# Kernel optimization log

Hardware: AMD Instinct MI355X
Metric: run time of the kernel (lower is better)

The kernel has to match this reference:

```python
import jax, jax.numpy as jnp
import numpy as np

B, T, D, H = 4, 2048, 1024, 64

def setup_inputs() -> dict:
    key = jax.random.key(0)
    kx, kq, kk, kv = jax.random.split(key, 4)
    s = 1.0 / np.sqrt(D)
    return {
        "x": jax.random.normal(kx, (B, T, D), dtype=jnp.float32),
        "Wq": jax.random.normal(kq, (D, H), dtype=jnp.float32) * s,
        "Wk": jax.random.normal(kk, (D, H), dtype=jnp.float32) * s,
        "Wv": jax.random.normal(kv, (D, H), dtype=jnp.float32) * s,
    }

def reference(x, Wq, Wk, Wv):
    # q,k,v: [B,T,H]
    q = jnp.einsum('btd,dh->bth', x, Wq)
    k = jnp.einsum('btd,dh->bth', x, Wk)
    v = jnp.einsum('btd,dh->bth', x, Wv)
    scale = jnp.asarray(H, x.dtype) ** -0.5
    wei = jnp.einsum('bqh,bkh->bqk', q, k) * scale  # [B,T,T]
    Tlen = x.shape[1]
    causal = jnp.tril(jnp.ones((Tlen, Tlen), dtype=bool))
    wei = jnp.where(causal, wei, -jnp.inf)
    attn = jax.nn.softmax(wei, axis=-1)
    return jnp.einsum('bqk,bkh->bqh', attn, v)
```

## Files before the change

### kernel.cpp

```cpp
#include <hip/hip_runtime.h>
#include <hip/hip_bf16.h>
#include <math.h>

#define Bb   4
#define Tlen 2048
#define Dd   1024
#define Hh   64
#define NROWS 8192
#define NQ   32
#define NC   4

typedef short bf16x8 __attribute__((ext_vector_type(8)));
typedef float f32x4  __attribute__((ext_vector_type(4)));

__device__ __forceinline__ unsigned short f2b(float f) {
    unsigned u = __float_as_uint(f);
    unsigned r = u + 0x7FFFu + ((u >> 16) & 1u);
    return (unsigned short)(r >> 16);
}
__device__ __forceinline__ unsigned pk2(float a, float b) {
    __hip_bfloat162 h = __float22bfloat162_rn(make_float2(a, b));
    return *reinterpret_cast<unsigned*>(&h);
}

__global__ __launch_bounds__(256) void wtrans_kernel(
    const float* __restrict__ Wq, const float* __restrict__ Wk,
    const float* __restrict__ Wv, unsigned short* __restrict__ wfrag)
{
    const int s = blockIdx.x * 256 + threadIdx.x;
    const int f   = s / 768;
    const int rem = s % 768;
    const int nb  = rem >> 6;
    const int lane = rem & 63;
    const int g = lane >> 4, qr = lane & 15;
    const int n = nb * 16 + qr;
    const int wsel = n >> 6, h = n & 63;
    const float* W = (wsel == 0) ? Wq : (wsel == 1) ? Wk : Wv;
    const int k0 = (f >> 1) * 64 + (f & 1) * 32 + g * 8;
    unsigned short tmp[8];
    #pragma unroll
    for (int j = 0; j < 8; ++j) tmp[j] = f2b(W[(size_t)(k0 + j) * Hh + h]);
    *(bf16x8*)(wfrag + (size_t)s * 8) = *(const bf16x8*)tmp;
}

__global__ __launch_bounds__(256) void proj_kernel(
    const float* __restrict__ x, const unsigned short* __restrict__ wfrag,
    unsigned short* __restrict__ qw, unsigned short* __restrict__ kw,
    unsigned short* __restrict__ vw)
{
    __shared__ unsigned short xs[2][32 * 64];

    const int rb   = blockIdx.x * 32;
    const int tid  = threadIdx.x;
    const int wv   = tid >> 6;
    const int lane = tid & 63;
    const int qr   = lane & 15;
    const int g    = lane >> 4;

    const int xr = tid >> 3, xc8 = tid & 7;
    const float* xg0 = x + (size_t)(rb + xr) * Dd + xc8 * 8;

    const unsigned short* wp = wfrag + ((size_t)(wv * 3) * 64 + lane) * 8;

    f32x4 acc[6] = {};

    float4 px0 = *(const float4*)(xg0 + 0);
    float4 px1 = *(const float4*)(xg0 + 4);

    #pragma unroll
    for (int t = 0; t < 16; ++t) {
        const int cur = t & 1;
        {
            union { unsigned u[4]; bf16x8 v; } p8;
            p8.u[0] = pk2(px0.x, px0.y);
            p8.u[1] = pk2(px0.z, px0.w);
            p8.u[2] = pk2(px1.x, px1.y);
            p8.u[3] = pk2(px1.z, px1.w);
            *(bf16x8*)(&xs[cur][xr * 64 + ((xc8 ^ (xr & 7)) << 3)]) = p8.v;
        }
        __syncthreads();

        if (t < 15) {
            px0 = *(const float4*)(xg0 + (t + 1) * 64 + 0);
            px1 = *(const float4*)(xg0 + (t + 1) * 64 + 4);
        }

        #pragma unroll
        for (int ks = 0; ks < 2; ++ks) {
            const int f = t * 2 + ks;
            bf16x8 b0 = *(const bf16x8*)(wp + (size_t)(f * 12 + 0) * 512);
            bf16x8 b1 = *(const bf16x8*)(wp + (size_t)(f * 12 + 1) * 512);
            bf16x8 b2 = *(const bf16x8*)(wp + (size_t)(f * 12 + 2) * 512);
            #pragma unroll
            for (int mf = 0; mf < 2; ++mf) {
                const int arow = mf * 16 + qr;
                const bf16x8 a = *(const bf16x8*)(
                    &xs[cur][arow * 64 + (((ks * 4 + g) ^ (arow & 7)) << 3)]);
                acc[mf * 3 + 0] = __builtin_amdgcn_mfma_f32_16x16x32_bf16(a, b0, acc[mf * 3 + 0], 0, 0, 0);
                acc[mf * 3 + 1] = __builtin_amdgcn_mfma_f32_16x16x32_bf16(a, b1, acc[mf * 3 + 1], 0, 0, 0);
                acc[mf * 3 + 2] = __builtin_amdgcn_mfma_f32_16x16x32_bf16(a, b2, acc[mf * 3 + 2], 0, 0, 0);
            }
        }
        __syncthreads();
    }

    #pragma unroll
    for (int mf = 0; mf < 2; ++mf) {
        #pragma unroll
        for (int nf = 0; nf < 3; ++nf) {
            const int n = wv * 48 + nf * 16 + qr;
            const int wsel = n >> 6, h = n & 63;
            unsigned short* out = (wsel == 0) ? qw : (wsel == 1) ? kw : vw;
            const f32x4 ov = acc[mf * 3 + nf];
            #pragma unroll
            for (int r = 0; r < 4; ++r)
                out[(size_t)(rb + mf * 16 + 4 * g + r) * Hh + h] = f2b(ov[r]);
        }
    }
}

#define XSTR 72
#define VSTR 40
__global__ __launch_bounds__(256) void attn_kernel(
    const unsigned short* __restrict__ qw, const unsigned short* __restrict__ kw,
    const unsigned short* __restrict__ vw,
    float* __restrict__ part_O, float* __restrict__ part_ml)
{
    __shared__ unsigned short ks_s[32 * XSTR];
    __shared__ unsigned short vt_s[64 * VSTR];

    const int qt = (NQ - 1) - blockIdx.x;
    const int ci = blockIdx.y;
    const int b  = blockIdx.z;
    const int tid = threadIdx.x;
    const int wv = tid >> 6, lane = tid & 63;
    const int qr = lane & 15, g = lane >> 4;

    const int ntk = 2 * qt + 2;
    const int tpc = (ntk + NC - 1) / NC;
    const int t0  = ci * tpc;
    const int t1  = (ntk < t0 + tpc) ? ntk : (t0 + tpc);

    const size_t base = (size_t)b * Tlen * Hh;
    const int qrow = qt * 64 + wv * 16 + qr;

    const bf16x8 qf0 = *(const bf16x8*)(qw + base + (size_t)qrow * Hh + 8 * g);
    const bf16x8 qf1 = *(const bf16x8*)(qw + base + (size_t)qrow * Hh + 32 + 8 * g);

    f32x4 o0 = {}, o1 = {}, o2 = {}, o3 = {};
    float m = -INFINITY, l = 0.f;

    for (int kt = t0; kt < t1; ++kt) {
        const int j0 = kt * 32;
        __syncthreads();
        {
            const int row = tid >> 3, cg = tid & 7;
            const bf16x8 k8 = *(const bf16x8*)(kw + base + (size_t)(j0 + row) * Hh + cg * 8);
            *(bf16x8*)(&ks_s[row * XSTR + ((cg ^ (row & 3)) << 3)]) = k8;
            const bf16x8 v8 = *(const bf16x8*)(vw + base + (size_t)(j0 + row) * Hh + cg * 8);
            #pragma unroll
            for (int u = 0; u < 8; ++u) {
                const int c = cg * 8 + u;
                const int jx = row ^ (((c >> 3) & 3) << 3);
                vt_s[c * VSTR + jx] = ((const unsigned short*)&v8)[u];
            }
        }
        __syncthreads();

        f32x4 a0 = {}, a1 = {};
        {
            const int sw = (g ^ (qr & 3)) << 3;
            bf16x8 kf;
            kf = *(const bf16x8*)(&ks_s[qr * XSTR + sw]);
            a0 = __builtin_amdgcn_mfma_f32_16x16x32_bf16(kf, qf0, a0, 0, 0, 0);
            kf = *(const bf16x8*)(&ks_s[qr * XSTR + 32 + sw]);
            a0 = __builtin_amdgcn_mfma_f32_16x16x32_bf16(kf, qf1, a0, 0, 0, 0);
            kf = *(const bf16x8*)(&ks_s[(16 + qr) * XSTR + sw]);
            a1 = __builtin_amdgcn_mfma_f32_16x16x32_bf16(kf, qf0, a1, 0, 0, 0);
            kf = *(const bf16x8*)(&ks_s[(16 + qr) * XSTR + 32 + sw]);
            a1 = __builtin_amdgcn_mfma_f32_16x16x32_bf16(kf, qf1, a1, 0, 0, 0);
        }

        float p[8];
        float tm = -INFINITY;
        #pragma unroll
        for (int jf = 0; jf < 2; ++jf) {
            #pragma unroll
            for (int r = 0; r < 4; ++r) {
                const int jg = j0 + jf * 16 + 4 * g + r;
                float s = ((jf == 0) ? a0[r] : a1[r]) * 0.125f;
                s = (jg > qrow) ? -INFINITY : s;
                p[jf * 4 + r] = s;
                tm = fmaxf(tm, s);
            }
        }
        tm = fmaxf(tm, __shfl_xor(tm, 16));
        tm = fmaxf(tm, __shfl_xor(tm, 32));
        const float mnew  = fmaxf(m, tm);
        const float alpha = (m == -INFINITY) ? 0.f : __expf(m - mnew);
        float psum = 0.f;
        #pragma unroll
        for (int i = 0; i < 8; ++i) {
            const float pv = (p[i] == -INFINITY) ? 0.f : __expf(p[i] - mnew);
            p[i] = pv; psum += pv;
        }
        psum += __shfl_xor(psum, 16);
        psum += __shfl_xor(psum, 32);
        l = l * alpha + psum;
        m = mnew;

        const float ar0 = __shfl(alpha, 4 * g + 0);
        const float ar1 = __shfl(alpha, 4 * g + 1);
        const float ar2 = __shfl(alpha, 4 * g + 2);
        const float ar3 = __shfl(alpha, 4 * g + 3);
        o0[0] *= ar0; o0[1] *= ar1; o0[2] *= ar2; o0[3] *= ar3;
        o1[0] *= ar0; o1[1] *= ar1; o1[2] *= ar2; o1[3] *= ar3;
        o2[0] *= ar0; o2[1] *= ar1; o2[2] *= ar2; o2[3] *= ar3;
        o3[0] *= ar0; o3[1] *= ar1; o3[2] *= ar2; o3[3] *= ar3;

        unsigned pw[4];
        pw[0] = f2b(p[0]) | ((unsigned)f2b(p[1]) << 16);
        pw[1] = f2b(p[2]) | ((unsigned)f2b(p[3]) << 16);
        pw[2] = f2b(p[4]) | ((unsigned)f2b(p[5]) << 16);
        pw[3] = f2b(p[6]) | ((unsigned)f2b(p[7]) << 16);
        union PU { unsigned u[4]; bf16x8 v; } pu;
        #pragma unroll
        for (int w = 0; w < 4; ++w) {
            const int gp  = 2 * g + (w >> 1);
            const int src = 16 * (gp & 3) + qr;
            const unsigned t0s = __shfl(pw[0 + (w & 1)], src);
            const unsigned t1s = __shfl(pw[2 + (w & 1)], src);
            pu.u[w] = (gp & 4) ? t1s : t0s;
        }
        const bf16x8 pa = pu.v;

        {
            int cb = qr;
            bf16x8 vf = *(const bf16x8*)(&vt_s[cb * VSTR + 8 * (g ^ ((cb >> 3) & 3))]);
            o0 = __builtin_amdgcn_mfma_f32_16x16x32_bf16(pa, vf, o0, 0, 0, 0);
            cb = 16 + qr;
            vf = *(const bf16x8*)(&vt_s[cb * VSTR + 8 * (g ^ ((cb >> 3) & 3))]);
            o1 = __builtin_amdgcn_mfma_f32_16x16x32_bf16(pa, vf, o1, 0, 0, 0);
            cb = 32 + qr;
            vf = *(const bf16x8*)(&vt_s[cb * VSTR + 8 * (g ^ ((cb >> 3) & 3))]);
            o2 = __builtin_amdgcn_mfma_f32_16x16x32_bf16(pa, vf, o2, 0, 0, 0);
            cb = 48 + qr;
            vf = *(const bf16x8*)(&vt_s[cb * VSTR + 8 * (g ^ ((cb >> 3) & 3))]);
            o3 = __builtin_amdgcn_mfma_f32_16x16x32_bf16(pa, vf, o3, 0, 0, 0);
        }
    }

    const int blin = (b * NQ + qt) * NC + ci;
    float* po = part_O + (size_t)blin * 4096;
    #pragma unroll
    for (int nf = 0; nf < 4; ++nf) {
        const f32x4 ov = (nf == 0) ? o0 : (nf == 1) ? o1 : (nf == 2) ? o2 : o3;
        #pragma unroll
        for (int r = 0; r < 4; ++r)
            po[(size_t)(wv * 16 + 4 * g + r) * 64 + nf * 16 + qr] = ov[r];
    }
    if (g == 0) {
        part_ml[(size_t)blin * 128 + wv * 16 + qr]      = m;
        part_ml[(size_t)blin * 128 + 64 + wv * 16 + qr] = l;
    }
}

__global__ __launch_bounds__(256) void merge_kernel(
    const float* __restrict__ part_O, const float* __restrict__ part_ml,
    float* __restrict__ out)
{
    const int idx = blockIdx.x * 256 + threadIdx.x;
    const int row = idx >> 6;
    const int c   = idx & 63;
    const int b   = row >> 11;
    const int t   = row & 2047;
    const int qt  = t >> 6;
    const int qq  = t & 63;
    const int bl0 = (b * NQ + qt) * NC;

    float M = -INFINITY;
    #pragma unroll
    for (int i = 0; i < NC; ++i) {
        const float lvi = part_ml[(size_t)(bl0 + i) * 128 + 64 + qq];
        if (lvi > 0.f) M = fmaxf(M, part_ml[(size_t)(bl0 + i) * 128 + qq]);
    }
    float num = 0.f, den = 0.f;
    #pragma unroll
    for (int i = 0; i < NC; ++i) {
        const float lvi = part_ml[(size_t)(bl0 + i) * 128 + 64 + qq];
        if (lvi > 0.f) {
            const float wgt = __expf(part_ml[(size_t)(bl0 + i) * 128 + qq] - M);
            num += wgt * part_O[(size_t)(bl0 + i) * 4096 + (size_t)qq * 64 + c];
            den += wgt * lvi;
        }
    }
    out[(size_t)row * 64 + c] = num / den;
}

extern "C" void kernel_launch(void* const* d_in, const int* in_sizes, int n_in,
                              void* d_out, int out_size, void* d_ws, size_t ws_size,
                              hipStream_t stream) {
    const float* x  = (const float*)d_in[0];
    const float* Wq = (const float*)d_in[1];
    const float* Wk = (const float*)d_in[2];
    const float* Wv = (const float*)d_in[3];
    float* outp = (float*)d_out;

    unsigned short* wfrag = (unsigned short*)d_ws;
    unsigned short* qw = wfrag + 192 * 1024;
    unsigned short* kw = qw + NROWS * Hh;
    unsigned short* vw = kw + NROWS * Hh;
    float* part_O  = (float*)(vw + NROWS * Hh);
    float* part_ml = part_O + (size_t)(Bb * NQ * NC) * 4096;

    wtrans_kernel<<<dim3(96), 256, 0, stream>>>(Wq, Wk, Wv, wfrag);
    proj_kernel<<<dim3(NROWS / 32), 256, 0, stream>>>(x, wfrag, qw, kw, vw);
    attn_kernel<<<dim3(NQ, NC, Bb), 256, 0, stream>>>(qw, kw, vw, part_O, part_ml);
    merge_kernel<<<dim3((NROWS * Hh) / 256), 256, 0, stream>>>(part_O, part_ml, outp);
}
```

Baseline: 49.34 us.

## Give each wave a private x tile in projection, dropping block barriers

The projection kernel now handles 16 rows per block instead of 32, which doubles the grid. Each wave loads and converts its own copy of the x tile into a private LDS slice, so both __syncthreads per k-step go away. The cost is that every x row is fetched four times, once per wave, which relies on cache hits to keep global traffic down. Each wave now carries three accumulators instead of six.

```diff
diff --git a/kernel.cpp b/kernel.cpp
--- a/kernel.cpp
+++ b/kernel.cpp
@@ -48,74 +48,73 @@
     unsigned short* __restrict__ qw, unsigned short* __restrict__ kw,
     unsigned short* __restrict__ vw)
 {
-    __shared__ unsigned short xs[2][32 * 64];
-
-    const int rb   = blockIdx.x * 32;
+    __shared__ unsigned short xs[4][16 * 64];
+
+    const int rt   = blockIdx.x;
     const int tid  = threadIdx.x;
     const int wv   = tid >> 6;
     const int lane = tid & 63;
     const int qr   = lane & 15;
     const int g    = lane >> 4;
 
-    const int xr = tid >> 3, xc8 = tid & 7;
-    const float* xg0 = x + (size_t)(rb + xr) * Dd + xc8 * 8;
+    const int xr8 = lane >> 3, xc8 = lane & 7;
+    const float* xg0 = x + (size_t)(rt * 16 + xr8) * Dd + xc8 * 8;
+    const float* xg1 = x + (size_t)(rt * 16 + 8 + xr8) * Dd + xc8 * 8;
+    const int wrow0 = xr8,     wsw0 = (xc8 ^ (wrow0 & 7)) << 3;
+    const int wrow1 = 8 + xr8, wsw1 = (xc8 ^ (wrow1 & 7)) << 3;
 
     const unsigned short* wp = wfrag + ((size_t)(wv * 3) * 64 + lane) * 8;
 
-    f32x4 acc[6] = {};
-
-    float4 px0 = *(const float4*)(xg0 + 0);
-    float4 px1 = *(const float4*)(xg0 + 4);
+    f32x4 acc[3] = {};
+
+    float4 pa0 = *(const float4*)(xg0 + 0);
+    float4 pa1 = *(const float4*)(xg0 + 4);
+    float4 pb0 = *(const float4*)(xg1 + 0);
+    float4 pb1 = *(const float4*)(xg1 + 4);
 
     #pragma unroll
     for (int t = 0; t < 16; ++t) {
-        const int cur = t & 1;
         {
-            union { unsigned u[4]; bf16x8 v; } p8;
-            p8.u[0] = pk2(px0.x, px0.y);
-            p8.u[1] = pk2(px0.z, px0.w);
-            p8.u[2] = pk2(px1.x, px1.y);
-            p8.u[3] = pk2(px1.z, px1.w);
-            *(bf16x8*)(&xs[cur][xr * 64 + ((xc8 ^ (xr & 7)) << 3)]) = p8.v;
-        }
-        __syncthreads();
+            union { unsigned u[4]; bf16x8 v; } w0, w1;
+            w0.u[0] = pk2(pa0.x, pa0.y); w0.u[1] = pk2(pa0.z, pa0.w);
+            w0.u[2] = pk2(pa1.x, pa1.y); w0.u[3] = pk2(pa1.z, pa1.w);
+            w1.u[0] = pk2(pb0.x, pb0.y); w1.u[1] = pk2(pb0.z, pb0.w);
+            w1.u[2] = pk2(pb1.x, pb1.y); w1.u[3] = pk2(pb1.z, pb1.w);
+            *(bf16x8*)(&xs[wv][wrow0 * 64 + wsw0]) = w0.v;
+            *(bf16x8*)(&xs[wv][wrow1 * 64 + wsw1]) = w1.v;
+        }
 
         if (t < 15) {
-            px0 = *(const float4*)(xg0 + (t + 1) * 64 + 0);
-            px1 = *(const float4*)(xg0 + (t + 1) * 64 + 4);
+            const int k1 = (t + 1) * 64;
+            pa0 = *(const float4*)(xg0 + k1 + 0);
+            pa1 = *(const float4*)(xg0 + k1 + 4);
+            pb0 = *(const float4*)(xg1 + k1 + 0);
+            pb1 = *(const float4*)(xg1 + k1 + 4);
         }
 
         #pragma unroll
         for (int ks = 0; ks < 2; ++ks) {
             const int f = t * 2 + ks;
-            bf16x8 b0 = *(const bf16x8*)(wp + (size_t)(f * 12 + 0) * 512);
-            bf16x8 b1 = *(const bf16x8*)(wp + (size_t)(f * 12 + 1) * 512);
-            bf16x8 b2 = *(const bf16x8*)(wp + (size_t)(f * 12 + 2) * 512);
-            #pragma unroll
-            for (int mf = 0; mf < 2; ++mf) {
-                const int arow = mf * 16 + qr;
-                const bf16x8 a = *(const bf16x8*)(
-                    &xs[cur][arow * 64 + (((ks * 4 + g) ^ (arow & 7)) << 3)]);
-                acc[mf * 3 + 0] = __builtin_amdgcn_mfma_f32_16x16x32_bf16(a, b0, acc[mf * 3 + 0], 0, 0, 0);
-                acc[mf * 3 + 1] = __builtin_amdgcn_mfma_f32_16x16x32_bf16(a, b1, acc[mf * 3 + 1], 0, 0, 0);
-                acc[mf * 3 + 2] = __builtin_amdgcn_mfma_f32_16x16x32_bf16(a, b2, acc[mf * 3 + 2], 0, 0, 0);
-            }
-        }
-        __syncthreads();
-    }
-
-    #pragma unroll
-    for (int mf = 0; mf < 2; ++mf) {
-        #pragma unroll
-        for (int nf = 0; nf < 3; ++nf) {
-            const int n = wv * 48 + nf * 16 + qr;
-            const int wsel = n >> 6, h = n & 63;
-            unsigned short* out = (wsel == 0) ? qw : (wsel == 1) ? kw : vw;
-            const f32x4 ov = acc[mf * 3 + nf];
-            #pragma unroll
-            for (int r = 0; r < 4; ++r)
-                out[(size_t)(rb + mf * 16 + 4 * g + r) * Hh + h] = f2b(ov[r]);
-        }
+            const int kg = ks * 4 + g;
+            const bf16x8 a = *(const bf16x8*)(
+                &xs[wv][qr * 64 + ((kg ^ (qr & 7)) << 3)]);
+            const bf16x8 b0 = *(const bf16x8*)(wp + (size_t)(f * 12 + 0) * 512);
+            const bf16x8 b1 = *(const bf16x8*)(wp + (size_t)(f * 12 + 1) * 512);
+            const bf16x8 b2 = *(const bf16x8*)(wp + (size_t)(f * 12 + 2) * 512);
+            acc[0] = __builtin_amdgcn_mfma_f32_16x16x32_bf16(a, b0, acc[0], 0, 0, 0);
+            acc[1] = __builtin_amdgcn_mfma_f32_16x16x32_bf16(a, b1, acc[1], 0, 0, 0);
+            acc[2] = __builtin_amdgcn_mfma_f32_16x16x32_bf16(a, b2, acc[2], 0, 0, 0);
+        }
+    }
+
+    #pragma unroll
+    for (int nf = 0; nf < 3; ++nf) {
+        const int n = wv * 48 + nf * 16 + qr;
+        const int wsel = n >> 6, h = n & 63;
+        unsigned short* out = (wsel == 0) ? qw : (wsel == 1) ? kw : vw;
+        #pragma unroll
+        for (int r = 0; r < 4; ++r)
+            out[(size_t)(rt * 16 + 4 * g + r) * Hh + h] = f2b(acc[nf][r]);
     }
 }
 
@@ -314,7 +313,7 @@
     float* part_ml = part_O + (size_t)(Bb * NQ * NC) * 4096;
 
     wtrans_kernel<<<dim3(96), 256, 0, stream>>>(Wq, Wk, Wv, wfrag);
-    proj_kernel<<<dim3(NROWS / 32), 256, 0, stream>>>(x, wfrag, qw, kw, vw);
+    proj_kernel<<<dim3(NROWS / 16), 256, 0, stream>>>(x, wfrag, qw, kw, vw);
     attn_kernel<<<dim3(NQ, NC, Bb), 256, 0, stream>>>(qw, kw, vw, part_O, part_ml);
     merge_kernel<<<dim3((NROWS * Hh) / 256), 256, 0, stream>>>(part_O, part_ml, outp);
 }
```

Measured after the change: 50.90 us. 1.03x slower.

## Fuse split-KV merge into attention via atomic tickets, prefetch K/V, double splits

Applied to the files above, without the earlier changes.

Drops the separate merge kernel. The last attention block to finish each query tile, found through an atomic ticket counter that wtrans resets, now combines the partial results and writes the output. It also doubles the number of KV splits per query tile to put more blocks on the GPU. It prefetches the next K/V tile into registers so the global loads overlap compute. The costs are more partial buffers, serialized merge work in the last block, and reliance on the workspace being large enough for the tickets.

```diff
diff --git a/kernel.cpp b/kernel.cpp
--- a/kernel.cpp
+++ b/kernel.cpp
@@ -8,7 +8,7 @@
 #define Hh   64
 #define NROWS 8192
 #define NQ   32
-#define NC   4
+#define NC   8
 
 typedef short bf16x8 __attribute__((ext_vector_type(8)));
 typedef float f32x4  __attribute__((ext_vector_type(4)));
@@ -25,9 +25,11 @@
 
 __global__ __launch_bounds__(256) void wtrans_kernel(
     const float* __restrict__ Wq, const float* __restrict__ Wk,
-    const float* __restrict__ Wv, unsigned short* __restrict__ wfrag)
+    const float* __restrict__ Wv, unsigned short* __restrict__ wfrag,
+    int* __restrict__ tickets)
 {
     const int s = blockIdx.x * 256 + threadIdx.x;
+    if (s < Bb * NQ) tickets[s] = 0;
     const int f   = s / 768;
     const int rem = s % 768;
     const int nb  = rem >> 6;
@@ -124,10 +126,12 @@
 __global__ __launch_bounds__(256) void attn_kernel(
     const unsigned short* __restrict__ qw, const unsigned short* __restrict__ kw,
     const unsigned short* __restrict__ vw,
-    float* __restrict__ part_O, float* __restrict__ part_ml)
+    float* __restrict__ part_O, float* __restrict__ part_ml,
+    int* __restrict__ tickets, float* __restrict__ out)
 {
     __shared__ unsigned short ks_s[32 * XSTR];
     __shared__ unsigned short vt_s[64 * VSTR];
+    __shared__ int tk_s;
 
     const int qt = (NQ - 1) - blockIdx.x;
     const int ci = blockIdx.y;
@@ -150,22 +154,33 @@
     f32x4 o0 = {}, o1 = {}, o2 = {}, o3 = {};
     float m = -INFINITY, l = 0.f;
 
+    const int srow = tid >> 3, scg = tid & 7;
+    const unsigned short* kbase = kw + base + (size_t)srow * Hh + scg * 8;
+    const unsigned short* vbase = vw + base + (size_t)srow * Hh + scg * 8;
+    bf16x8 k8 = {}, v8 = {};
+    if (t0 < t1) {
+        k8 = *(const bf16x8*)(kbase + (size_t)t0 * 32 * Hh);
+        v8 = *(const bf16x8*)(vbase + (size_t)t0 * 32 * Hh);
+    }
+
     for (int kt = t0; kt < t1; ++kt) {
         const int j0 = kt * 32;
         __syncthreads();
         {
-            const int row = tid >> 3, cg = tid & 7;
-            const bf16x8 k8 = *(const bf16x8*)(kw + base + (size_t)(j0 + row) * Hh + cg * 8);
-            *(bf16x8*)(&ks_s[row * XSTR + ((cg ^ (row & 3)) << 3)]) = k8;
-            const bf16x8 v8 = *(const bf16x8*)(vw + base + (size_t)(j0 + row) * Hh + cg * 8);
+            *(bf16x8*)(&ks_s[srow * XSTR + ((scg ^ (srow & 3)) << 3)]) = k8;
             #pragma unroll
             for (int u = 0; u < 8; ++u) {
-                const int c = cg * 8 + u;
-                const int jx = row ^ (((c >> 3) & 3) << 3);
+                const int c = scg * 8 + u;
+                const int jx = srow ^ (((c >> 3) & 3) << 3);
                 vt_s[c * VSTR + jx] = ((const unsigned short*)&v8)[u];
             }
         }
         __syncthreads();
+
+        if (kt + 1 < t1) {
+            k8 = *(const bf16x8*)(kbase + (size_t)(kt + 1) * 32 * Hh);
+            v8 = *(const bf16x8*)(vbase + (size_t)(kt + 1) * 32 * Hh);
+        }
 
         f32x4 a0 = {}, a1 = {};
         {
@@ -263,38 +278,44 @@
         part_ml[(size_t)blin * 128 + wv * 16 + qr]      = m;
         part_ml[(size_t)blin * 128 + 64 + wv * 16 + qr] = l;
     }
-}
-
-__global__ __launch_bounds__(256) void merge_kernel(
-    const float* __restrict__ part_O, const float* __restrict__ part_ml,
-    float* __restrict__ out)
-{
-    const int idx = blockIdx.x * 256 + threadIdx.x;
-    const int row = idx >> 6;
-    const int c   = idx & 63;
-    const int b   = row >> 11;
-    const int t   = row & 2047;
-    const int qt  = t >> 6;
-    const int qq  = t & 63;
-    const int bl0 = (b * NQ + qt) * NC;
-
-    float M = -INFINITY;
-    #pragma unroll
-    for (int i = 0; i < NC; ++i) {
-        const float lvi = part_ml[(size_t)(bl0 + i) * 128 + 64 + qq];
-        if (lvi > 0.f) M = fmaxf(M, part_ml[(size_t)(bl0 + i) * 128 + qq]);
-    }
-    float num = 0.f, den = 0.f;
-    #pragma unroll
-    for (int i = 0; i < NC; ++i) {
-        const float lvi = part_ml[(size_t)(bl0 + i) * 128 + 64 + qq];
-        if (lvi > 0.f) {
-            const float wgt = __expf(part_ml[(size_t)(bl0 + i) * 128 + qq] - M);
-            num += wgt * part_O[(size_t)(bl0 + i) * 4096 + (size_t)qq * 64 + c];
-            den += wgt * lvi;
-        }
-    }
-    out[(size_t)row * 64 + c] = num / den;
+
+    if (tid == 0) {
+        __threadfence();
+        tk_s = atomicAdd(&tickets[b * NQ + qt], 1);
+    }
+    __syncthreads();
+    if (tk_s == NC - 1) {
+        __threadfence();
+        const int row = tid >> 2;
+        const int c0  = (tid & 3) * 16;
+        const int bl0 = (b * NQ + qt) * NC;
+
+        float mv[NC], lv[NC], wgt[NC];
+        float M = -INFINITY;
+        #pragma unroll
+        for (int i = 0; i < NC; ++i) {
+            mv[i] = part_ml[(size_t)(bl0 + i) * 128 + row];
+            lv[i] = part_ml[(size_t)(bl0 + i) * 128 + 64 + row];
+            if (lv[i] > 0.f) M = fmaxf(M, mv[i]);
+        }
+        float den = 0.f;
+        #pragma unroll
+        for (int i = 0; i < NC; ++i) {
+            wgt[i] = (lv[i] > 0.f) ? __expf(mv[i] - M) : 0.f;
+            den += wgt[i] * lv[i];
+        }
+        const float inv = 1.f / den;
+        #pragma unroll
+        for (int c = 0; c < 16; ++c) {
+            float num = 0.f;
+            #pragma unroll
+            for (int i = 0; i < NC; ++i) {
+                if (lv[i] > 0.f)
+                    num += wgt[i] * part_O[(size_t)(bl0 + i) * 4096 + (size_t)row * 64 + c0 + c];
+            }
+            out[(size_t)(b * Tlen + qt * 64 + row) * Hh + c0 + c] = num * inv;
+        }
+    }
 }
 
 extern "C" void kernel_launch(void* const* d_in, const int* in_sizes, int n_in,
@@ -312,9 +333,9 @@
     unsigned short* vw = kw + NROWS * Hh;
     float* part_O  = (float*)(vw + NROWS * Hh);
     float* part_ml = part_O + (size_t)(Bb * NQ * NC) * 4096;
-
-    wtrans_kernel<<<dim3(96), 256, 0, stream>>>(Wq, Wk, Wv, wfrag);
+    int*   tickets = (int*)(part_ml + (size_t)(Bb * NQ * NC) * 128);
+
+    wtrans_kernel<<<dim3(96), 256, 0, stream>>>(Wq, Wk, Wv, wfrag, tickets);
     proj_kernel<<<dim3(NROWS / 32), 256, 0, stream>>>(x, wfrag, qw, kw, vw);
-    attn_kernel<<<dim3(NQ, NC, Bb), 256, 0, stream>>>(qw, kw, vw, part_O, part_ml);
-    merge_kernel<<<dim3((NROWS * Hh) / 256), 256, 0, stream>>>(part_O, part_ml, outp);
-}
+    attn_kernel<<<dim3(NQ, NC, Bb), 256, 0, stream>>>(qw, kw, vw, part_O, part_ml, tickets, outp);
+}
```

Result: slower. 150.0 us (+204.0%).

## Double-buffer shared tiles in projection and attention kernels with one barrier

Applied to the files above, without the earlier changes.

Both the projection and attention kernels now keep two shared-memory buffers. The next tile is loaded from global memory into registers before the current tile's MFMA work and stored to the alternate buffer afterward. This removes one __syncthreads per iteration and hides global load latency behind compute. Shared memory use doubles and register pressure rises from the prefetched values, which could reduce occupancy.

```diff
diff --git a/kernel.cpp b/kernel.cpp
--- a/kernel.cpp
+++ b/kernel.cpp
@@ -59,30 +59,30 @@
 
     const int xr = tid >> 3, xc8 = tid & 7;
     const float* xg0 = x + (size_t)(rb + xr) * Dd + xc8 * 8;
+    const int wsw = ((xc8 ^ (xr & 7)) << 3);
 
     const unsigned short* wp = wfrag + ((size_t)(wv * 3) * 64 + lane) * 8;
 
     f32x4 acc[6] = {};
 
-    float4 px0 = *(const float4*)(xg0 + 0);
-    float4 px1 = *(const float4*)(xg0 + 4);
-
+    {
+        const float4 u0 = *(const float4*)(xg0 + 0);
+        const float4 u1 = *(const float4*)(xg0 + 4);
+        union { unsigned u[4]; bf16x8 v; } p8;
+        p8.u[0] = pk2(u0.x, u0.y); p8.u[1] = pk2(u0.z, u0.w);
+        p8.u[2] = pk2(u1.x, u1.y); p8.u[3] = pk2(u1.z, u1.w);
+        *(bf16x8*)(&xs[0][xr * 64 + wsw]) = p8.v;
+    }
+
+    float4 n0, n1;
     #pragma unroll
     for (int t = 0; t < 16; ++t) {
         const int cur = t & 1;
-        {
-            union { unsigned u[4]; bf16x8 v; } p8;
-            p8.u[0] = pk2(px0.x, px0.y);
-            p8.u[1] = pk2(px0.z, px0.w);
-            p8.u[2] = pk2(px1.x, px1.y);
-            p8.u[3] = pk2(px1.z, px1.w);
-            *(bf16x8*)(&xs[cur][xr * 64 + ((xc8 ^ (xr & 7)) << 3)]) = p8.v;
-        }
         __syncthreads();
 
         if (t < 15) {
-            px0 = *(const float4*)(xg0 + (t + 1) * 64 + 0);
-            px1 = *(const float4*)(xg0 + (t + 1) * 64 + 4);
+            n0 = *(const float4*)(xg0 + (t + 1) * 64 + 0);
+            n1 = *(const float4*)(xg0 + (t + 1) * 64 + 4);
         }
 
         #pragma unroll
@@ -101,7 +101,13 @@
                 acc[mf * 3 + 2] = __builtin_amdgcn_mfma_f32_16x16x32_bf16(a, b2, acc[mf * 3 + 2], 0, 0, 0);
             }
         }
-        __syncthreads();
+
+        if (t < 15) {
+            union { unsigned u[4]; bf16x8 v; } p8;
+            p8.u[0] = pk2(n0.x, n0.y); p8.u[1] = pk2(n0.z, n0.w);
+            p8.u[2] = pk2(n1.x, n1.y); p8.u[3] = pk2(n1.z, n1.w);
+            *(bf16x8*)(&xs[cur ^ 1][xr * 64 + wsw]) = p8.v;
+        }
     }
 
     #pragma unroll
@@ -126,8 +132,8 @@
     const unsigned short* __restrict__ vw,
     float* __restrict__ part_O, float* __restrict__ part_ml)
 {
-    __shared__ unsigned short ks_s[32 * XSTR];
-    __shared__ unsigned short vt_s[64 * VSTR];
+    __shared__ unsigned short ks_s[2][32 * XSTR];
+    __shared__ unsigned short vt_s[2][64 * VSTR];
 
     const int qt = (NQ - 1) - blockIdx.x;
     const int ci = blockIdx.y;
@@ -150,34 +156,45 @@
     f32x4 o0 = {}, o1 = {}, o2 = {}, o3 = {};
     float m = -INFINITY, l = 0.f;
 
+    const int srow = tid >> 3, scg = tid & 7;
+    const unsigned short* kbase = kw + base + (size_t)srow * Hh + scg * 8;
+    const unsigned short* vbase = vw + base + (size_t)srow * Hh + scg * 8;
+    const int ksw = ((scg ^ (srow & 3)) << 3);
+
+    if (t0 < t1) {
+        const bf16x8 k8 = *(const bf16x8*)(kbase + (size_t)t0 * 32 * Hh);
+        const bf16x8 v8 = *(const bf16x8*)(vbase + (size_t)t0 * 32 * Hh);
+        *(bf16x8*)(&ks_s[0][srow * XSTR + ksw]) = k8;
+        #pragma unroll
+        for (int u = 0; u < 8; ++u) {
+            const int c = scg * 8 + u;
+            const int jx = srow ^ (((c >> 3) & 3) << 3);
+            vt_s[0][c * VSTR + jx] = ((const unsigned short*)&v8)[u];
+        }
+    }
+
+    bf16x8 k8n, v8n;
     for (int kt = t0; kt < t1; ++kt) {
+        const int cur = (kt - t0) & 1;
         const int j0 = kt * 32;
         __syncthreads();
-        {
-            const int row = tid >> 3, cg = tid & 7;
-            const bf16x8 k8 = *(const bf16x8*)(kw + base + (size_t)(j0 + row) * Hh + cg * 8);
-            *(bf16x8*)(&ks_s[row * XSTR + ((cg ^ (row & 3)) << 3)]) = k8;
-            const bf16x8 v8 = *(const bf16x8*)(vw + base + (size_t)(j0 + row) * Hh + cg * 8);
-            #pragma unroll
-            for (int u = 0; u < 8; ++u) {
-                const int c = cg * 8 + u;
-                const int jx = row ^ (((c >> 3) & 3) << 3);
-                vt_s[c * VSTR + jx] = ((const unsigned short*)&v8)[u];
-            }
-        }
-        __syncthreads();
+
+        if (kt + 1 < t1) {
+            k8n = *(const bf16x8*)(kbase + (size_t)(kt + 1) * 32 * Hh);
+            v8n = *(const bf16x8*)(vbase + (size_t)(kt + 1) * 32 * Hh);
+        }
 
         f32x4 a0 = {}, a1 = {};
         {
             const int sw = (g ^ (qr & 3)) << 3;
             bf16x8 kf;
-            kf = *(const bf16x8*)(&ks_s[qr * XSTR + sw]);
+            kf = *(const bf16x8*)(&ks_s[cur][qr * XSTR + sw]);
             a0 = __builtin_amdgcn_mfma_f32_16x16x32_bf16(kf, qf0, a0, 0, 0, 0);
-            kf = *(const bf16x8*)(&ks_s[qr * XSTR + 32 + sw]);
+            kf = *(const bf16x8*)(&ks_s[cur][qr * XSTR + 32 + sw]);
             a0 = __builtin_amdgcn_mfma_f32_16x16x32_bf16(kf, qf1, a0, 0, 0, 0);
-            kf = *(const bf16x8*)(&ks_s[(16 + qr) * XSTR + sw]);
+            kf = *(const bf16x8*)(&ks_s[cur][(16 + qr) * XSTR + sw]);
             a1 = __builtin_amdgcn_mfma_f32_16x16x32_bf16(kf, qf0, a1, 0, 0, 0);
-            kf = *(const bf16x8*)(&ks_s[(16 + qr) * XSTR + 32 + sw]);
+            kf = *(const bf16x8*)(&ks_s[cur][(16 + qr) * XSTR + 32 + sw]);
             a1 = __builtin_amdgcn_mfma_f32_16x16x32_bf16(kf, qf1, a1, 0, 0, 0);
         }
 
@@ -236,17 +253,27 @@
 
         {
             int cb = qr;
-            bf16x8 vf = *(const bf16x8*)(&vt_s[cb * VSTR + 8 * (g ^ ((cb >> 3) & 3))]);
+            bf16x8 vf = *(const bf16x8*)(&vt_s[cur][cb * VSTR + 8 * (g ^ ((cb >> 3) & 3))]);
             o0 = __builtin_amdgcn_mfma_f32_16x16x32_bf16(pa, vf, o0, 0, 0, 0);
             cb = 16 + qr;
-            vf = *(const bf16x8*)(&vt_s[cb * VSTR + 8 * (g ^ ((cb >> 3) & 3))]);
+            vf = *(const bf16x8*)(&vt_s[cur][cb * VSTR + 8 * (g ^ ((cb >> 3) & 3))]);
             o1 = __builtin_amdgcn_mfma_f32_16x16x32_bf16(pa, vf, o1, 0, 0, 0);
             cb = 32 + qr;
-            vf = *(const bf16x8*)(&vt_s[cb * VSTR + 8 * (g ^ ((cb >> 3) & 3))]);
+            vf = *(const bf16x8*)(&vt_s[cur][cb * VSTR + 8 * (g ^ ((cb >> 3) & 3))]);
             o2 = __builtin_amdgcn_mfma_f32_16x16x32_bf16(pa, vf, o2, 0, 0, 0);
             cb = 48 + qr;
-            vf = *(const bf16x8*)(&vt_s[cb * VSTR + 8 * (g ^ ((cb >> 3) & 3))]);
+            vf = *(const bf16x8*)(&vt_s[cur][cb * VSTR + 8 * (g ^ ((cb >> 3) & 3))]);
             o3 = __builtin_amdgcn_mfma_f32_16x16x32_bf16(pa, vf, o3, 0, 0, 0);
+        }
+
+        if (kt + 1 < t1) {
+            *(bf16x8*)(&ks_s[cur ^ 1][srow * XSTR + ksw]) = k8n;
+            #pragma unroll
+            for (int u = 0; u < 8; ++u) {
+                const int c = scg * 8 + u;
+                const int jx = srow ^ (((c >> 3) & 3) << 3);
+                vt_s[cur ^ 1][c * VSTR + jx] = ((const unsigned short*)&v8n)[u];
+            }
         }
     }
 
```

Measured after the change: 51.78 us. 4.9% more time.
